# Performance work log

Measured on AMD Instinct MI355X. Metric: run time of the kernel, lower is better.

The kernel has to match this reference:

```python
import jax, jax.numpy as jnp
import numpy as np

E = 8            # num_local_experts
K = 2            # top-2 gate
CAP_FACTOR = 1.0 # tutel default capacity factor


def setup_inputs() -> dict:
    key = jax.random.key(0)
    k0, k1, k2, k3 = jax.random.split(key, 4)
    B, N, D, H = 8, 8192, 512, 512
    s = 0.02
    return {
        "x": jax.random.normal(k0, (B, N, D), jnp.float32),
        "Wg": jax.random.normal(k1, (D, E), jnp.float32) * s,
        "W1": jax.random.normal(k2, (E, D, H), jnp.float32) * s,
        "b1": jnp.zeros((E, H), jnp.float32),
        "W2": jax.random.normal(k3, (E, H, D), jnp.float32) * s,
        "b2": jnp.zeros((E, D), jnp.float32),
    }


def _moe(x, Wg, W1, b1, W2, b2):
    B, N, D = x.shape
    T = B * N
    xt = x.reshape(T, D)
    # --- gating (Top2Gate): softmax over experts, take top-2, renormalize ---
    gates = jax.nn.softmax(xt @ Wg, axis=-1)            # [T, E]
    topw, topi = jax.lax.top_k(gates, K)                # [T, K]
    topw = topw / jnp.sum(topw, axis=-1, keepdims=True)
    # --- capacity & per-expert positions (k=0 assignments fill first) ---
    C = int(np.ceil(K * T / E * CAP_FACTOR))
    onehot = jax.nn.one_hot(topi, E, dtype=jnp.int32)   # [T, K, E]
    flat = onehot.transpose(1, 0, 2).reshape(K * T, E)  # k-major order
    pos_flat = jnp.cumsum(flat, axis=0) - 1             # running count per expert
    pos = (pos_flat * flat).sum(-1).reshape(K, T).T     # [T, K] slot within expert
    keep = (pos < C).astype(xt.dtype)                   # [T, K] capacity drop mask
    # --- dispatch: scatter tokens into [E, C, D] expert buffers ---
    ei = topi.reshape(-1)                               # [T*K]
    pi = jnp.clip(pos, 0, C - 1).reshape(-1)            # [T*K]
    vals = (xt[:, None, :] * keep[:, :, None]).reshape(T * K, D)
    buf = jnp.zeros((E, C, D), xt.dtype).at[ei, pi].add(vals)
    # --- per-expert FFN (identity activation) ---
    h = jnp.einsum('ecd,edh->ech', buf, W1) + b1[:, None, :]
    out = jnp.einsum('ech,ehd->ecd', h, W2) + b2[:, None, :]
    # --- combine: gather expert outputs, weight, sum over k ---
    gathered = out[ei, pi].reshape(T, K, D)
    y = jnp.sum(gathered * (topw * keep)[:, :, None], axis=1)
    return y.reshape(B, N, D)


def reference(x, Wg, W1, b1, W2, b2):
    y = _moe(x, Wg, W1, b1, W2, b2)        # [B, N, D]
    return jax.nn.log_softmax(jnp.sum(y, axis=2), axis=1)  # [B, N]
```

## Files before the change

kernel.cpp:

```cpp
#include <hip/hip_runtime.h>

#define T_TOK 65536
#define DDIM 512
#define NEXP 8
#define CAP 16384

__device__ inline float wave_sum(float v) {
#pragma unroll
  for (int m = 1; m < 64; m <<= 1) v += __shfl_xor(v, m, 64);
  return v;
}

template <int CTRL>
__device__ __forceinline__ float dppf(float v) {
  return __int_as_float(
      __builtin_amdgcn_mov_dpp(__float_as_int(v), CTRL, 0xf, 0xf, true));
}
__device__ __forceinline__ void pl32swap(float& a, float& b) {
  asm("v_permlane32_swap_b32 %0, %1" : "+v"(a), "+v"(b));
}
__device__ __forceinline__ void pl16swap(float& a, float& b) {
  asm("v_permlane16_swap_b32 %0, %1" : "+v"(a), "+v"(b));
}

__global__ void k_w2s(const float* __restrict__ W2, const float* __restrict__ Wg,
                      float* __restrict__ w2s, float* __restrict__ wT) {
  if (blockIdx.x < 1024) {
    int w = threadIdx.x >> 6, lane = threadIdx.x & 63;
    int row = blockIdx.x * 4 + w;
    const float* p = W2 + (size_t)row * 512;
    float sum = 0.f;
#pragma unroll
    for (int j = 0; j < 8; ++j) sum += p[lane + j * 64];
    sum = wave_sum(sum);
    if (lane == 0) w2s[row] = sum;
  } else {
    int i = (blockIdx.x - 1024) * 256 + threadIdx.x;
    int e = i >> 9, d = i & 511;
    wT[i] = Wg[d * 8 + e];
  }
}

__global__ void k_v_beta(const float* __restrict__ W1, const float* __restrict__ b1,
                         const float* __restrict__ b2, const float* __restrict__ w2s,
                         float* __restrict__ wT, float* __restrict__ beta) {
  int w = threadIdx.x >> 6, lane = threadIdx.x & 63;
  if (blockIdx.x < 1024) {
    int rid = blockIdx.x * 4 + w;
    int e = rid >> 9, d = rid & 511;
    const float* p = W1 + (size_t)rid * 512;
    const float* q = w2s + e * 512;
    float sum = 0.f;
#pragma unroll
    for (int j = 0; j < 8; ++j) { int h = lane + j * 64; sum += p[h] * q[h]; }
    sum = wave_sum(sum);
    if (lane == 0) wT[(size_t)(8 + e) * 512 + d] = sum;
  } else {
#pragma unroll
    for (int r = 0; r < 2; ++r) {
      int e = w + r * 4;
      float sum = 0.f;
#pragma unroll
      for (int j = 0; j < 8; ++j) {
        int i = lane + j * 64;
        sum += b1[e * 512 + i] * w2s[e * 512 + i] + b2[e * 512 + i];
      }
      sum = wave_sum(sum);
      if (lane == 0) beta[e] = sum;
    }
  }
}

__global__ __launch_bounds__(1024, 4) void k_dots(const float* __restrict__ x,
                                                  const float* __restrict__ wT,
                                                  const float* __restrict__ beta,
                                                  float4* __restrict__ wd,
                                                  int* __restrict__ epk,
                                                  int* __restrict__ hist) {
  __shared__ float sD[256 * 17];
  __shared__ int c0[8], c1[8];
  const int tid = threadIdx.x;
  const int lane = tid & 63;
  const int wave = tid >> 6;
  const int wo = wave & 1;
  const int tset = wave >> 1;
  const int tbase = blockIdx.x * 256 + tset * 32;

  float w[8][8];
#pragma unroll
  for (int o = 0; o < 8; ++o) {
    const float* wp = wT + (size_t)(wo * 8 + o) * 512 + 8 * lane;
    float4 wa = *reinterpret_cast<const float4*>(wp);
    float4 wb = *reinterpret_cast<const float4*>(wp + 4);
    w[o][0] = wa.x; w[o][1] = wa.y; w[o][2] = wa.z; w[o][3] = wa.w;
    w[o][4] = wb.x; w[o][5] = wb.y; w[o][6] = wb.z; w[o][7] = wb.w;
  }

  const bool kb3 = (lane & 8) != 0;
  const float* xb = x + (size_t)tbase * 512 + 8 * lane;

  auto proc = [&](int r, float4 x0, float4 x1) {
    float p[8];
#pragma unroll
    for (int o = 0; o < 8; ++o)
      p[o] = x0.x * w[o][0] + x0.y * w[o][1] + x0.z * w[o][2] + x0.w * w[o][3] +
             x1.x * w[o][4] + x1.y * w[o][5] + x1.z * w[o][6] + x1.w * w[o][7];
    float a[4];
#pragma unroll
    for (int j = 0; j < 4; ++j) {
      float u = p[j], v = p[j + 4];
      pl32swap(u, v);
      a[j] = u + v;
    }
    float b[2];
#pragma unroll
    for (int j = 0; j < 2; ++j) {
      float u = a[j], v = a[j + 2];
      pl16swap(u, v);
      b[j] = u + v;
    }
    float snd = kb3 ? b[0] : b[1];
    float kp  = kb3 ? b[1] : b[0];
    float c = kp + dppf<0x128>(snd);
    c += dppf<0x141>(c);
    c += dppf<0x4E>(c);
    c += dppf<0xB1>(c);
    if ((lane & 7) == 0)
      sD[(tset * 32 + r) * 17 + wo * 8 + (lane >> 3)] = c;
  };

  float4 s00, s01, s10, s11, s20, s21, s30, s31;
  const float* q;
  q = xb;        s00 = *reinterpret_cast<const float4*>(q); s01 = *reinterpret_cast<const float4*>(q + 4);
  q = xb + 512;  s10 = *reinterpret_cast<const float4*>(q); s11 = *reinterpret_cast<const float4*>(q + 4);
  q = xb + 1024; s20 = *reinterpret_cast<const float4*>(q); s21 = *reinterpret_cast<const float4*>(q + 4);

#pragma unroll
  for (int r = 0; r < 32; r += 4) {
    q = xb + (size_t)(r + 3) * 512;
    s30 = *reinterpret_cast<const float4*>(q); s31 = *reinterpret_cast<const float4*>(q + 4);
    proc(r, s00, s01);
    if (r + 4 < 32) {
      q = xb + (size_t)(r + 4) * 512;
      s00 = *reinterpret_cast<const float4*>(q); s01 = *reinterpret_cast<const float4*>(q + 4);
    }
    proc(r + 1, s10, s11);
    if (r + 5 < 32) {
      q = xb + (size_t)(r + 5) * 512;
      s10 = *reinterpret_cast<const float4*>(q); s11 = *reinterpret_cast<const float4*>(q + 4);
    }
    proc(r + 2, s20, s21);
    if (r + 6 < 32) {
      q = xb + (size_t)(r + 6) * 512;
      s20 = *reinterpret_cast<const float4*>(q); s21 = *reinterpret_cast<const float4*>(q + 4);
    }
    proc(r + 3, s30, s31);
  }

  __syncthreads();
  if (tid < 8) { c0[tid] = 0; c1[tid] = 0; }
  __syncthreads();
  if (tid < 256) {
    const int t = blockIdx.x * 256 + tid;
    float l[8], dv[8];
#pragma unroll
    for (int e = 0; e < 8; ++e) { l[e] = sD[tid * 17 + e]; dv[e] = sD[tid * 17 + 8 + e]; }
    int e1 = 0; float v1 = l[0];
#pragma unroll
    for (int e = 1; e < 8; ++e) if (l[e] > v1) { v1 = l[e]; e1 = e; }
    int e2 = 0; float v2 = -3.4e38f;
#pragma unroll
    for (int e = 0; e < 8; ++e) if (e != e1 && l[e] > v2) { v2 = l[e]; e2 = e; }
    float wexp = expf(v2 - v1);
    float w1 = 1.f / (1.f + wexp);
    float w2 = wexp * w1;
    float d1 = 0.f, d2 = 0.f;
#pragma unroll
    for (int e = 0; e < 8; ++e) {
      d1 = (e == e1) ? dv[e] : d1;
      d2 = (e == e2) ? dv[e] : d2;
    }
    float4 o; o.x = w1; o.y = w2; o.z = d1 + beta[e1]; o.w = d2 + beta[e2];
    wd[t] = o;
    epk[t] = e1 | (e2 << 8);
    atomicAdd(&c0[e1], 1);
    atomicAdd(&c1[e2], 1);
  }
  __syncthreads();
  if (tid < 8) {
    hist[blockIdx.x * 8 + tid] = c0[tid];
    hist[(256 + blockIdx.x) * 8 + tid] = c1[tid];
  }
}

__global__ __launch_bounds__(512) void k_scan(const int* __restrict__ hist,
                                              int* __restrict__ off) {
  __shared__ int sH[4096];
  __shared__ int sT[512];
  int tid = threadIdx.x;
#pragma unroll
  for (int i = tid; i < 4096; i += 512) sH[i] = hist[i];
  __syncthreads();
  int e = tid & 7, g = tid >> 3;
  int run = 0;
#pragma unroll
  for (int i = g * 8; i < g * 8 + 8; ++i) {
    int cv = sH[i * 8 + e]; sH[i * 8 + e] = run; run += cv;
  }
  sT[tid] = run;
  __syncthreads();
  int inc = run;
#pragma unroll
  for (int st = 1; st < 64; st <<= 1) {
    int add = (g >= st) ? sT[tid - st * 8] : 0;
    __syncthreads();
    inc += add;
    sT[tid] = inc;
    __syncthreads();
  }
  int exc = inc - run;
#pragma unroll
  for (int i = g * 8; i < g * 8 + 8; ++i) sH[i * 8 + e] += exc;
  __syncthreads();
#pragma unroll
  for (int i = tid; i < 4096; i += 512) off[i] = sH[i];
}

__global__ void k_keep(const int* __restrict__ epk, const float4* __restrict__ wd,
                       const int* __restrict__ off, float* __restrict__ s) {
  __shared__ int sC0[32], sC1[32];
  int tid = threadIdx.x, lane = tid & 63, w = tid >> 6;
  int t = blockIdx.x * 256 + tid;
  int ep = epk[t]; int e1 = ep & 255, e2 = ep >> 8;
  unsigned long long lt = (1ull << lane) - 1ull;
  int wr0 = 0, wr1 = 0;
#pragma unroll
  for (int e = 0; e < 8; ++e) {
    unsigned long long m0 = __ballot(e1 == e);
    unsigned long long m1 = __ballot(e2 == e);
    if (e == e1) wr0 = __popcll(m0 & lt);
    if (e == e2) wr1 = __popcll(m1 & lt);
    if (lane == 0) { sC0[w * 8 + e] = __popcll(m0); sC1[w * 8 + e] = __popcll(m1); }
  }
  __syncthreads();
  int woff0 = 0, woff1 = 0;
  for (int wp = 0; wp < 4; ++wp) {
    if (wp < w) { woff0 += sC0[wp * 8 + e1]; woff1 += sC1[wp * 8 + e2]; }
  }
  int b = blockIdx.x;
  int pos0 = off[b * 8 + e1] + woff0 + wr0;
  int pos1 = off[(256 + b) * 8 + e2] + woff1 + wr1;
  float4 v = wd[t];
  float sv = 0.f;
  if (pos0 < CAP) sv += v.x * v.z;
  if (pos1 < CAP) sv += v.y * v.w;
  s[t] = sv;
}

__global__ __launch_bounds__(1024) void k_lsm(const float* __restrict__ s,
                                              float* __restrict__ out) {
  __shared__ float sRa[16], sRb[16];
  int tid = threadIdx.x, lane = tid & 63, w = tid >> 6;
  size_t base = (size_t)blockIdx.x * 8192;
  float v[8];
#pragma unroll
  for (int j = 0; j < 8; ++j) v[j] = s[base + tid + j * 1024];
  float mx = v[0];
#pragma unroll
  for (int j = 1; j < 8; ++j) mx = fmaxf(mx, v[j]);
#pragma unroll
  for (int m = 1; m < 64; m <<= 1) mx = fmaxf(mx, __shfl_xor(mx, m, 64));
  if (lane == 0) sRa[w] = mx;
  __syncthreads();
#pragma unroll
  for (int i = 0; i < 16; ++i) mx = fmaxf(mx, sRa[i]);
  float sum = 0.f;
#pragma unroll
  for (int j = 0; j < 8; ++j) sum += expf(v[j] - mx);
#pragma unroll
  for (int m = 1; m < 64; m <<= 1) sum += __shfl_xor(sum, m, 64);
  if (lane == 0) sRb[w] = sum;
  __syncthreads();
  float tot = 0.f;
#pragma unroll
  for (int i = 0; i < 16; ++i) tot += sRb[i];
  float lse = logf(tot);
#pragma unroll
  for (int j = 0; j < 8; ++j) out[base + tid + j * 1024] = v[j] - mx - lse;
}

extern "C" void kernel_launch(void* const* d_in, const int* in_sizes, int n_in,
                              void* d_out, int out_size, void* d_ws, size_t ws_size,
                              hipStream_t stream) {
  const float* x  = (const float*)d_in[0];
  const float* Wg = (const float*)d_in[1];
  const float* W1 = (const float*)d_in[2];
  const float* b1 = (const float*)d_in[3];
  const float* W2 = (const float*)d_in[4];
  const float* b2 = (const float*)d_in[5];
  float* out = (float*)d_out;
  char* ws = (char*)d_ws;

  float*  w2s  = (float*)(ws);
  float*  wT   = (float*)(ws + (16u << 10));
  float*  beta = (float*)(ws + (48u << 10));
  float4* wd   = (float4*)(ws + (64u << 10));
  int*    epk  = (int*)(ws + (64u << 10) + (1u << 20));
  int*    hist = (int*)(ws + (64u << 10) + (1u << 20) + (256u << 10));
  int*    offa = (int*)(ws + (64u << 10) + (1u << 20) + (272u << 10));
  float*  s    = (float*)(ws + (64u << 10) + (1u << 20) + (288u << 10));

  hipLaunchKernelGGL(k_w2s,    dim3(1040), dim3(256),  0, stream, W2, Wg, w2s, wT);
  hipLaunchKernelGGL(k_v_beta, dim3(1025), dim3(256),  0, stream, W1, b1, b2, w2s, wT, beta);
  hipLaunchKernelGGL(k_dots,   dim3(256),  dim3(1024), 0, stream, x, wT, beta, wd, epk, hist);
  hipLaunchKernelGGL(k_scan,   dim3(1),    dim3(512),  0, stream, hist, offa);
  hipLaunchKernelGGL(k_keep,   dim3(256),  dim3(256),  0, stream, epk, wd, offa, s);
  hipLaunchKernelGGL(k_lsm,    dim3(8),    dim3(1024), 0, stream, s, out);
}
```

Measured before the change: 48.88 us.

## Fuse scan, keep-mask and log-softmax kernels into one tail kernel

Replaces the three final kernels (single-block histogram scan, per-token capacity keep, per-row log-softmax) with one 8-block kernel. Each block redundantly recomputes the full 4096-entry exclusive scan in shared memory, then computes the keep-masked scores for its 8192 tokens and does the log-softmax in registers. This removes two kernel launches and the global round-trips for the offsets and scores. In exchange the scan work is duplicated across 8 blocks, and the keep phase now runs on only 8 blocks with a barrier per iteration instead of 256 blocks.

```diff
diff --git a/kernel.cpp b/kernel.cpp
--- a/kernel.cpp
+++ b/kernel.cpp
@@ -193,84 +193,82 @@
   }
 }
 
-__global__ __launch_bounds__(512) void k_scan(const int* __restrict__ hist,
-                                              int* __restrict__ off) {
+__global__ __launch_bounds__(1024) void k_tail(const int* __restrict__ hist,
+                                               const int* __restrict__ epk,
+                                               const float4* __restrict__ wd,
+                                               float* __restrict__ out) {
   __shared__ int sH[4096];
-  __shared__ int sT[512];
-  int tid = threadIdx.x;
-#pragma unroll
-  for (int i = tid; i < 4096; i += 512) sH[i] = hist[i];
-  __syncthreads();
-  int e = tid & 7, g = tid >> 3;
-  int run = 0;
-#pragma unroll
-  for (int i = g * 8; i < g * 8 + 8; ++i) {
-    int cv = sH[i * 8 + e]; sH[i * 8 + e] = run; run += cv;
-  }
-  sT[tid] = run;
-  __syncthreads();
-  int inc = run;
-#pragma unroll
-  for (int st = 1; st < 64; st <<= 1) {
-    int add = (g >= st) ? sT[tid - st * 8] : 0;
+  __shared__ int sT[1024];
+  __shared__ int sC0[4][32], sC1[4][32];
+  __shared__ float sRa[16], sRb[16];
+  const int tid = threadIdx.x;
+
+  for (int i = tid; i < 4096; i += 1024) sH[i] = hist[i];
+  __syncthreads();
+  {
+    int e = tid & 7, g = tid >> 3;
+    int run = 0;
+#pragma unroll
+    for (int i = g * 4; i < g * 4 + 4; ++i) {
+      int cv = sH[i * 8 + e]; sH[i * 8 + e] = run; run += cv;
+    }
+    sT[tid] = run;
     __syncthreads();
-    inc += add;
-    sT[tid] = inc;
+    int inc = run;
+#pragma unroll
+    for (int st = 1; st < 128; st <<= 1) {
+      int add = (g >= st) ? sT[tid - st * 8] : 0;
+      __syncthreads();
+      inc += add;
+      sT[tid] = inc;
+      __syncthreads();
+    }
+    int exc = inc - run;
+#pragma unroll
+    for (int i = g * 4; i < g * 4 + 4; ++i) sH[i * 8 + e] += exc;
+  }
+  __syncthreads();
+
+  const int lane = tid & 63, wv = tid >> 6;
+  const int grp = wv >> 2, w = wv & 3;
+  const size_t base = (size_t)blockIdx.x * 8192;
+  float v[8];
+#pragma unroll
+  for (int j = 0; j < 8; ++j) {
+    int t = (int)base + j * 1024 + tid;
+    int ep = epk[t]; int e1 = ep & 255, e2 = ep >> 8;
+    unsigned long long lt = (1ull << lane) - 1ull;
+    int wr0 = 0, wr1 = 0;
+#pragma unroll
+    for (int ee = 0; ee < 8; ++ee) {
+      unsigned long long m0 = __ballot(e1 == ee);
+      unsigned long long m1 = __ballot(e2 == ee);
+      if (ee == e1) wr0 = __popcll(m0 & lt);
+      if (ee == e2) wr1 = __popcll(m1 & lt);
+      if (lane == 0) { sC0[grp][w * 8 + ee] = __popcll(m0); sC1[grp][w * 8 + ee] = __popcll(m1); }
+    }
     __syncthreads();
-  }
-  int exc = inc - run;
-#pragma unroll
-  for (int i = g * 8; i < g * 8 + 8; ++i) sH[i * 8 + e] += exc;
-  __syncthreads();
-#pragma unroll
-  for (int i = tid; i < 4096; i += 512) off[i] = sH[i];
-}
-
-__global__ void k_keep(const int* __restrict__ epk, const float4* __restrict__ wd,
-                       const int* __restrict__ off, float* __restrict__ s) {
-  __shared__ int sC0[32], sC1[32];
-  int tid = threadIdx.x, lane = tid & 63, w = tid >> 6;
-  int t = blockIdx.x * 256 + tid;
-  int ep = epk[t]; int e1 = ep & 255, e2 = ep >> 8;
-  unsigned long long lt = (1ull << lane) - 1ull;
-  int wr0 = 0, wr1 = 0;
-#pragma unroll
-  for (int e = 0; e < 8; ++e) {
-    unsigned long long m0 = __ballot(e1 == e);
-    unsigned long long m1 = __ballot(e2 == e);
-    if (e == e1) wr0 = __popcll(m0 & lt);
-    if (e == e2) wr1 = __popcll(m1 & lt);
-    if (lane == 0) { sC0[w * 8 + e] = __popcll(m0); sC1[w * 8 + e] = __popcll(m1); }
-  }
-  __syncthreads();
-  int woff0 = 0, woff1 = 0;
-  for (int wp = 0; wp < 4; ++wp) {
-    if (wp < w) { woff0 += sC0[wp * 8 + e1]; woff1 += sC1[wp * 8 + e2]; }
-  }
-  int b = blockIdx.x;
-  int pos0 = off[b * 8 + e1] + woff0 + wr0;
-  int pos1 = off[(256 + b) * 8 + e2] + woff1 + wr1;
-  float4 v = wd[t];
-  float sv = 0.f;
-  if (pos0 < CAP) sv += v.x * v.z;
-  if (pos1 < CAP) sv += v.y * v.w;
-  s[t] = sv;
-}
-
-__global__ __launch_bounds__(1024) void k_lsm(const float* __restrict__ s,
-                                              float* __restrict__ out) {
-  __shared__ float sRa[16], sRb[16];
-  int tid = threadIdx.x, lane = tid & 63, w = tid >> 6;
-  size_t base = (size_t)blockIdx.x * 8192;
-  float v[8];
-#pragma unroll
-  for (int j = 0; j < 8; ++j) v[j] = s[base + tid + j * 1024];
+    int woff0 = 0, woff1 = 0;
+#pragma unroll
+    for (int wp = 0; wp < 4; ++wp)
+      if (wp < w) { woff0 += sC0[grp][wp * 8 + e1]; woff1 += sC1[grp][wp * 8 + e2]; }
+    int b = t >> 8;
+    int pos0 = sH[b * 8 + e1] + woff0 + wr0;
+    int pos1 = sH[(256 + b) * 8 + e2] + woff1 + wr1;
+    float4 d = wd[t];
+    float sv = 0.f;
+    if (pos0 < CAP) sv += d.x * d.z;
+    if (pos1 < CAP) sv += d.y * d.w;
+    v[j] = sv;
+    __syncthreads();
+  }
+
   float mx = v[0];
 #pragma unroll
   for (int j = 1; j < 8; ++j) mx = fmaxf(mx, v[j]);
 #pragma unroll
   for (int m = 1; m < 64; m <<= 1) mx = fmaxf(mx, __shfl_xor(mx, m, 64));
-  if (lane == 0) sRa[w] = mx;
+  if (lane == 0) sRa[wv] = mx;
   __syncthreads();
 #pragma unroll
   for (int i = 0; i < 16; ++i) mx = fmaxf(mx, sRa[i]);
@@ -279,14 +277,14 @@
   for (int j = 0; j < 8; ++j) sum += expf(v[j] - mx);
 #pragma unroll
   for (int m = 1; m < 64; m <<= 1) sum += __shfl_xor(sum, m, 64);
-  if (lane == 0) sRb[w] = sum;
+  if (lane == 0) sRb[wv] = sum;
   __syncthreads();
   float tot = 0.f;
 #pragma unroll
   for (int i = 0; i < 16; ++i) tot += sRb[i];
   float lse = logf(tot);
 #pragma unroll
-  for (int j = 0; j < 8; ++j) out[base + tid + j * 1024] = v[j] - mx - lse;
+  for (int j = 0; j < 8; ++j) out[base + tid + (size_t)j * 1024] = v[j] - mx - lse;
 }
 
 extern "C" void kernel_launch(void* const* d_in, const int* in_sizes, int n_in,
@@ -307,13 +305,9 @@
   float4* wd   = (float4*)(ws + (64u << 10));
   int*    epk  = (int*)(ws + (64u << 10) + (1u << 20));
   int*    hist = (int*)(ws + (64u << 10) + (1u << 20) + (256u << 10));
-  int*    offa = (int*)(ws + (64u << 10) + (1u << 20) + (272u << 10));
-  float*  s    = (float*)(ws + (64u << 10) + (1u << 20) + (288u << 10));
 
   hipLaunchKernelGGL(k_w2s,    dim3(1040), dim3(256),  0, stream, W2, Wg, w2s, wT);
   hipLaunchKernelGGL(k_v_beta, dim3(1025), dim3(256),  0, stream, W1, b1, b2, w2s, wT, beta);
   hipLaunchKernelGGL(k_dots,   dim3(256),  dim3(1024), 0, stream, x, wT, beta, wd, epk, hist);
-  hipLaunchKernelGGL(k_scan,   dim3(1),    dim3(512),  0, stream, hist, offa);
-  hipLaunchKernelGGL(k_keep,   dim3(256),  dim3(256),  0, stream, epk, wd, offa, s);
-  hipLaunchKernelGGL(k_lsm,    dim3(8),    dim3(1024), 0, stream, s, out);
-}
+  hipLaunchKernelGGL(k_tail,   dim3(8),    dim3(1024), 0, stream, hist, epk, wd, out);
+}
```

Result: slower. 70.27 us (+43.8%).

## Split wave pair work along D instead of output columns in gate dot kernel

Applied to the files above, without the earlier changes.

Each wave pair now splits the 512-wide hidden dimension in half, and every wave computes all 16 outputs (8 gate logits plus 8 fused dot values) over its half. Each lane loads one float4 of x per row instead of two, and the two partial sums are added when the results are read back from shared memory. The change keeps the same register count for weights and makes each wave read a contiguous 1 KB half-row of x. In exchange it adds a deeper cross-lane reduction (more permlane/DPP steps), doubles the shared-memory buffer and adds extra LDS reads in the epilogue.

```diff
diff --git a/kernel.cpp b/kernel.cpp
--- a/kernel.cpp
+++ b/kernel.cpp
@@ -77,84 +77,76 @@
                                                   float4* __restrict__ wd,
                                                   int* __restrict__ epk,
                                                   int* __restrict__ hist) {
-  __shared__ float sD[256 * 17];
+  __shared__ float sD[2][256 * 17];
   __shared__ int c0[8], c1[8];
   const int tid = threadIdx.x;
   const int lane = tid & 63;
   const int wave = tid >> 6;
-  const int wo = wave & 1;
+  const int wp = wave & 1;
   const int tset = wave >> 1;
   const int tbase = blockIdx.x * 256 + tset * 32;
 
-  float w[8][8];
-#pragma unroll
-  for (int o = 0; o < 8; ++o) {
-    const float* wp = wT + (size_t)(wo * 8 + o) * 512 + 8 * lane;
-    float4 wa = *reinterpret_cast<const float4*>(wp);
-    float4 wb = *reinterpret_cast<const float4*>(wp + 4);
-    w[o][0] = wa.x; w[o][1] = wa.y; w[o][2] = wa.z; w[o][3] = wa.w;
-    w[o][4] = wb.x; w[o][5] = wb.y; w[o][6] = wb.z; w[o][7] = wb.w;
-  }
-
-  const bool kb3 = (lane & 8) != 0;
-  const float* xb = x + (size_t)tbase * 512 + 8 * lane;
-
-  auto proc = [&](int r, float4 x0, float4 x1) {
-    float p[8];
-#pragma unroll
-    for (int o = 0; o < 8; ++o)
-      p[o] = x0.x * w[o][0] + x0.y * w[o][1] + x0.z * w[o][2] + x0.w * w[o][3] +
-             x1.x * w[o][4] + x1.y * w[o][5] + x1.z * w[o][6] + x1.w * w[o][7];
-    float a[4];
-#pragma unroll
-    for (int j = 0; j < 4; ++j) {
-      float u = p[j], v = p[j + 4];
+  float4 w[16];
+#pragma unroll
+  for (int o = 0; o < 16; ++o)
+    w[o] = *reinterpret_cast<const float4*>(wT + (size_t)o * 512 + wp * 256 + 4 * lane);
+
+  const bool b3 = (lane & 8) != 0;
+  const bool b2l = (lane & 4) != 0;
+  const float* xb = x + (size_t)tbase * 512 + wp * 256 + 4 * lane;
+
+  auto proc = [&](int r, float4 x0) {
+    float p[16];
+#pragma unroll
+    for (int o = 0; o < 16; ++o)
+      p[o] = x0.x * w[o].x + x0.y * w[o].y + x0.z * w[o].z + x0.w * w[o].w;
+    float a[8];
+#pragma unroll
+    for (int j = 0; j < 8; ++j) {
+      float u = p[j], v = p[j + 8];
       pl32swap(u, v);
       a[j] = u + v;
     }
-    float b[2];
-#pragma unroll
-    for (int j = 0; j < 2; ++j) {
-      float u = a[j], v = a[j + 2];
+    float b[4];
+#pragma unroll
+    for (int j = 0; j < 4; ++j) {
+      float u = a[j], v = a[j + 4];
       pl16swap(u, v);
       b[j] = u + v;
     }
-    float snd = kb3 ? b[0] : b[1];
-    float kp  = kb3 ? b[1] : b[0];
-    float c = kp + dppf<0x128>(snd);
-    c += dppf<0x141>(c);
-    c += dppf<0x4E>(c);
-    c += dppf<0xB1>(c);
-    if ((lane & 7) == 0)
-      sD[(tset * 32 + r) * 17 + wo * 8 + (lane >> 3)] = c;
+    float c[2];
+#pragma unroll
+    for (int j = 0; j < 2; ++j) {
+      float snd = b3 ? b[j] : b[j + 2];
+      float kp  = b3 ? b[j + 2] : b[j];
+      c[j] = kp + dppf<0x128>(snd);
+    }
+    {
+      float snd = b2l ? c[0] : c[1];
+      float kp  = b2l ? c[1] : c[0];
+      float d = kp + dppf<0x141>(snd);
+      float e = d + dppf<0x4E>(d);
+      float f = e + dppf<0xB1>(e);
+      if ((lane & 3) == 0)
+        sD[wp][(tset * 32 + r) * 17 + (lane >> 2)] = f;
+    }
   };
 
-  float4 s00, s01, s10, s11, s20, s21, s30, s31;
-  const float* q;
-  q = xb;        s00 = *reinterpret_cast<const float4*>(q); s01 = *reinterpret_cast<const float4*>(q + 4);
-  q = xb + 512;  s10 = *reinterpret_cast<const float4*>(q); s11 = *reinterpret_cast<const float4*>(q + 4);
-  q = xb + 1024; s20 = *reinterpret_cast<const float4*>(q); s21 = *reinterpret_cast<const float4*>(q + 4);
+  float4 s0, s1, s2, s3;
+  s0 = *reinterpret_cast<const float4*>(xb);
+  s1 = *reinterpret_cast<const float4*>(xb + 512);
+  s2 = *reinterpret_cast<const float4*>(xb + 1024);
 
 #pragma unroll
   for (int r = 0; r < 32; r += 4) {
-    q = xb + (size_t)(r + 3) * 512;
-    s30 = *reinterpret_cast<const float4*>(q); s31 = *reinterpret_cast<const float4*>(q + 4);
-    proc(r, s00, s01);
-    if (r + 4 < 32) {
-      q = xb + (size_t)(r + 4) * 512;
-      s00 = *reinterpret_cast<const float4*>(q); s01 = *reinterpret_cast<const float4*>(q + 4);
-    }
-    proc(r + 1, s10, s11);
-    if (r + 5 < 32) {
-      q = xb + (size_t)(r + 5) * 512;
-      s10 = *reinterpret_cast<const float4*>(q); s11 = *reinterpret_cast<const float4*>(q + 4);
-    }
-    proc(r + 2, s20, s21);
-    if (r + 6 < 32) {
-      q = xb + (size_t)(r + 6) * 512;
-      s20 = *reinterpret_cast<const float4*>(q); s21 = *reinterpret_cast<const float4*>(q + 4);
-    }
-    proc(r + 3, s30, s31);
+    s3 = *reinterpret_cast<const float4*>(xb + (size_t)(r + 3) * 512);
+    proc(r, s0);
+    if (r + 4 < 32) s0 = *reinterpret_cast<const float4*>(xb + (size_t)(r + 4) * 512);
+    proc(r + 1, s1);
+    if (r + 5 < 32) s1 = *reinterpret_cast<const float4*>(xb + (size_t)(r + 5) * 512);
+    proc(r + 2, s2);
+    if (r + 6 < 32) s2 = *reinterpret_cast<const float4*>(xb + (size_t)(r + 6) * 512);
+    proc(r + 3, s3);
   }
 
   __syncthreads();
@@ -164,7 +156,10 @@
     const int t = blockIdx.x * 256 + tid;
     float l[8], dv[8];
 #pragma unroll
-    for (int e = 0; e < 8; ++e) { l[e] = sD[tid * 17 + e]; dv[e] = sD[tid * 17 + 8 + e]; }
+    for (int e = 0; e < 8; ++e) {
+      l[e]  = sD[0][tid * 17 + e]     + sD[1][tid * 17 + e];
+      dv[e] = sD[0][tid * 17 + 8 + e] + sD[1][tid * 17 + 8 + e];
+    }
     int e1 = 0; float v1 = l[0];
 #pragma unroll
     for (int e = 1; e < 8; ++e) if (l[e] > v1) { v1 = l[e]; e1 = e; }
```

Result: slower. 50.33 us (+3.0%).
